# Performance work log

Measured on AMD Instinct MI355X. Metric: run time of the kernel, lower is better.

The kernel has to match this reference:

```python
import jax, jax.numpy as jnp
import numpy as np

N = 100000
NFEAT = 128
NHID = 128
NCLASS = 40
E = 1600000
EPS = 1e-5


def _spmm(vals, src, dst, x, n):
    # y[dst] += vals * x[src]  (sparse adj @ x)
    return jax.ops.segment_sum(vals[:, None] * x[src], dst, num_segments=n)


def _bn(h, gamma, beta, rmean, rvar):
    # BatchNorm1d in eval mode (running statistics)
    return (h - rmean) * jax.lax.rsqrt(rvar + EPS) * gamma + beta


def setup_inputs() -> dict:
    key = jax.random.key(0)
    ks = jax.random.split(key, 24)
    inp = {
        'x': jax.random.normal(ks[0], (N, NFEAT), dtype=jnp.float32),
        'M': jax.random.uniform(ks[1], (N, 1), dtype=jnp.float32),
        'AM': jax.random.uniform(ks[2], (N, 1), dtype=jnp.float32),
        'srcZ': jax.random.randint(ks[3], (E,), 0, N, dtype=jnp.int32),
        'dstZ': jax.random.randint(ks[4], (E,), 0, N, dtype=jnp.int32),
        'valsZ': jax.random.uniform(ks[5], (E,), dtype=jnp.float32),
        'src': jax.random.randint(ks[6], (E,), 0, N, dtype=jnp.int32),
        'dst': jax.random.randint(ks[7], (E,), 0, N, dtype=jnp.int32),
        'vals': jax.random.uniform(ks[8], (E,), dtype=jnp.float32),
        # layer 0 (PaGConv) params
        'W0': jax.random.normal(ks[9], (NHID, NFEAT), dtype=jnp.float32) * (1.414 / np.sqrt(NFEAT)),
        'b0': jnp.zeros((NHID,), dtype=jnp.float32),
        'g0': jnp.ones((NHID,), dtype=jnp.float32),
        'be0': jnp.zeros((NHID,), dtype=jnp.float32),
        'rm0': jax.random.normal(ks[10], (NHID,), dtype=jnp.float32) * 0.1,
        'rv0': jax.random.uniform(ks[11], (NHID,), dtype=jnp.float32) + 0.5,
        # layer 1 (GConv) params
        'W1': jax.random.normal(ks[12], (NHID, NHID), dtype=jnp.float32) * (1.414 / np.sqrt(NHID)),
        'b1': jnp.zeros((NHID,), dtype=jnp.float32),
        'g1': jnp.ones((NHID,), dtype=jnp.float32),
        'be1': jnp.zeros((NHID,), dtype=jnp.float32),
        'rm1': jax.random.normal(ks[13], (NHID,), dtype=jnp.float32) * 0.1,
        'rv1': jax.random.uniform(ks[14], (NHID,), dtype=jnp.float32) + 0.5,
        # layer 2 (GConv) params
        'W2': jax.random.normal(ks[15], (NCLASS, NHID), dtype=jnp.float32) * (1.414 / np.sqrt(NHID)),
        'b2': jnp.zeros((NCLASS,), dtype=jnp.float32),
    }
    return inp


def reference(x, M, AM, srcZ, dstZ, valsZ, src, dst, vals,
              W0, b0, g0, be0, rm0, rv0,
              W1, b1, g1, be1, rm1, rv1,
              W2, b2):
    n = x.shape[0]
    # layer 0: PaGConv with adjZ: fc(spmm(adjZ, M*x) * AM), then BN + ReLU (dropout off in eval)
    h = _spmm(valsZ, srcZ, dstZ, M * x, n) * AM
    h = h @ W0.T + b0
    h = jax.nn.relu(_bn(h, g0, be0, rm0, rv0))
    # layer 1: GConv with adj: fc(spmm(adj, h)), then BN + ReLU
    h = _spmm(vals, src, dst, h, n)
    h = h @ W1.T + b1
    h = jax.nn.relu(_bn(h, g1, be1, rm1, rv1))
    # layer 2: GConv, then log_softmax
    h = _spmm(vals, src, dst, h, n)
    h = h @ W2.T + b2
    return jax.nn.log_softmax(h, axis=-1)
```

## Files before the change

kernel.cpp:

```cpp
#include <hip/hip_runtime.h>
#include <math.h>

#define NFEAT 128
#define NCLS 40
#define KSLOT 48
#define BINROWS 64
#define NBINMAX 1600
#define NBLKC 256
#define CHUNKMAX 6400
#define SEGC 7

typedef short bf16x8 __attribute__((ext_vector_type(8)));
typedef float f32x4 __attribute__((ext_vector_type(4)));

__device__ __forceinline__ float bf2f(unsigned int lo16) {
  return __uint_as_float((lo16 & 0xffffu) << 16);
}
__device__ __forceinline__ unsigned int f2bf(float x) {
  unsigned int u = __float_as_uint(x);
  return (u + 0x7fffu + ((u >> 16) & 1u)) >> 16;
}

__global__ void bn_prep(const float* b0, const float* g0, const float* be0,
                        const float* rm0, const float* rv0,
                        const float* b1, const float* g1, const float* be1,
                        const float* rm1, const float* rv1,
                        float* sc0, float* sh0, float* sc1, float* sh1) {
  int t = threadIdx.x;
  if (t < 128) {
    float s = g0[t] * rsqrtf(rv0[t] + 1e-5f);
    sc0[t] = s;
    sh0[t] = (b0[t] - rm0[t]) * s + be0[t];
  } else {
    int i = t - 128;
    float s = g1[i] * rsqrtf(rv1[i] + 1e-5f);
    sc1[i] = s;
    sh1[i] = (b1[i] - rm1[i]) * s + be1[i];
  }
}

__global__ void convert_xm(const float* __restrict__ x, const float* __restrict__ Mv,
                           unsigned short* __restrict__ xm, int n) {
  int i = blockIdx.x * 256 + threadIdx.x;
  if (i >= n * (NFEAT / 8)) return;
  int row = i >> 4;
  float m = Mv[row];
  const float4* p = (const float4*)(x + (size_t)i * 8);
  float4 v0 = p[0], v1 = p[1];
  unsigned int o0 = f2bf(v0.x * m) | (f2bf(v0.y * m) << 16);
  unsigned int o1 = f2bf(v0.z * m) | (f2bf(v0.w * m) << 16);
  unsigned int o2 = f2bf(v1.x * m) | (f2bf(v1.y * m) << 16);
  unsigned int o3 = f2bf(v1.z * m) | (f2bf(v1.w * m) << 16);
  ((uint4*)xm)[i] = make_uint4(o0, o1, o2, o3);
}

__global__ void convert_w(const float* __restrict__ W0, const float* __restrict__ W1,
                          unsigned short* __restrict__ Wb0, unsigned short* __restrict__ Wb1) {
  int i = blockIdx.x * 256 + threadIdx.x;
  const float* W = (i < 2048) ? W0 : W1;
  unsigned short* Wb = (i < 2048) ? Wb0 : Wb1;
  int j = (i < 2048) ? i : i - 2048;
  const float4* p = (const float4*)(W + (size_t)j * 8);
  float4 v0 = p[0], v1 = p[1];
  unsigned int o0 = f2bf(v0.x) | (f2bf(v0.y) << 16);
  unsigned int o1 = f2bf(v0.z) | (f2bf(v0.w) << 16);
  unsigned int o2 = f2bf(v1.x) | (f2bf(v1.y) << 16);
  unsigned int o3 = f2bf(v1.z) | (f2bf(v1.w) << 16);
  ((uint4*)Wb)[j] = make_uint4(o0, o1, o2, o3);
}

__global__ __launch_bounds__(256) void bin_sort_lds(
    const int* __restrict__ srcZ, const int* __restrict__ dstZ, const float* __restrict__ valsZ,
    const int* __restrict__ srcA, const int* __restrict__ dstA, const float* __restrict__ valsA,
    int2* __restrict__ DrmZ, int2* __restrict__ DrmA,
    int2* __restrict__ binsZ, int2* __restrict__ binsA, int E, int nbin, int chunk) {
  __shared__ int2 stage[CHUNKMAX];
  __shared__ int cur[NBINMAX];
  __shared__ int ps[256];
  const int t = threadIdx.x, k = blockIdx.x;
  const int a = blockIdx.y;
  const int* srcp = a ? srcA : srcZ;
  const int* dstp = a ? dstA : dstZ;
  const float* valp = a ? valsA : valsZ;
  int2* Drm = a ? DrmA : DrmZ;
  int2* binsOut = a ? binsA : binsZ;

  for (int i = t; i < nbin; i += 256) cur[i] = 0;
  __syncthreads();
  const int e0 = k * chunk, e1 = min(E, e0 + chunk);
#pragma unroll 4
  for (int e = e0 + t; e < e1; e += 256) atomicAdd(&cur[dstp[e] >> 6], 1);
  __syncthreads();
  int loc[SEGC], cnt[SEGC];
  int s = 0;
#pragma unroll
  for (int j = 0; j < SEGC; ++j) {
    int i = t * SEGC + j;
    int v = (i < nbin) ? cur[i] : 0;
    loc[j] = s; cnt[j] = v;
    s += v;
  }
  ps[t] = s;
  __syncthreads();
  for (int o = 1; o < 256; o <<= 1) {
    int x = (t >= o) ? ps[t - o] : 0;
    __syncthreads();
    ps[t] += x;
    __syncthreads();
  }
  int ex = ps[t] - s;
#pragma unroll
  for (int j = 0; j < SEGC; ++j) {
    int i = t * SEGC + j;
    if (i < nbin) {
      int o = ex + loc[j];
      Drm[(size_t)k * nbin + i] = make_int2(e0 + o, cnt[j]);
      cur[i] = o;
    }
  }
  __syncthreads();
#pragma unroll 2
  for (int e = e0 + t; e < e1; e += 256) {
    int d = dstp[e];
    int p = atomicAdd(&cur[d >> 6], 1);
    stage[p] = make_int2(srcp[e] | ((d & 63) << 17), __float_as_int(valp[e]));
  }
  __syncthreads();
  const int n = e1 - e0;
  for (int i = t; i < n; i += 256) binsOut[e0 + i] = stage[i];
}

__global__ __launch_bounds__(256) void transposeD(
    const int2* __restrict__ DrmZ, int2* __restrict__ DbmZ,
    const int2* __restrict__ DrmA, int2* __restrict__ DbmA, int nbin) {
  __shared__ int2 st[8][256];
  const int2* Drm = blockIdx.y ? DrmA : DrmZ;
  int2* Dbm = blockIdx.y ? DbmA : DbmZ;
  int t = threadIdx.x;
  int i0 = blockIdx.x * 8;
#pragma unroll
  for (int j = 0; j < 8; ++j) {
    int i = i0 + j;
    st[j][t] = (i < nbin) ? Drm[(size_t)t * nbin + i] : make_int2(0, 0);
  }
  __syncthreads();
  int j = t >> 5, ks = (t & 31) * 8;
  int i = i0 + j;
  if (i < nbin) {
    int2* q = &Dbm[(size_t)i * NBLKC + ks];
#pragma unroll
    for (int m = 0; m < 8; ++m) q[m] = st[j][ks + m];
  }
}

__device__ __forceinline__ void build_slots(const int2* __restrict__ Dbm,
                                            const int2* __restrict__ bins,
                                            int bin, int t,
                                            int2 (*slots)[KSLOT], int* cur) {
  if (t < BINROWS) cur[t] = 0;
  __syncthreads();
  int2 run = Dbm[(size_t)bin * NBLKC + t];
  for (int j = 0; j < run.y; ++j) {
    int2 en = bins[run.x + j];
    int row = (en.x >> 17) & 63;
    int p = atomicAdd(&cur[row], 1);
    if (p < KSLOT) slots[row][p] = make_int2(en.x & 0x1FFFF, en.y);
  }
  __syncthreads();
}

template <bool SCALE>
__global__ __launch_bounds__(256) void spmm128_bin(
    const int2* __restrict__ Dbm, const int2* __restrict__ bins,
    const unsigned short* __restrict__ X, const float* __restrict__ AM,
    unsigned short* __restrict__ Y, int n) {
  __shared__ int2 slots[BINROWS][KSLOT];
  __shared__ int cur[BINROWS];
  int t = threadIdx.x;
  build_slots(Dbm, bins, blockIdx.x, t, slots, cur);

  int wave = t >> 6, lane = t & 63;
  int half = lane >> 5, l32 = lane & 31;
  int row0 = blockIdx.x * BINROWS;

  for (int i = 0; i < 16; ++i) {
    int r = wave * 16 + i;
    int grow = row0 + r;
    if (grow >= n) break;
    int d = min(cur[r], KSLOT);
    int2 my = (lane < d) ? slots[r][lane] : make_int2(0, 0);
    int myc = my.x;
    float myw = __int_as_float(my.y);
    float s0 = 0.f, s1 = 0.f, s2 = 0.f, s3 = 0.f;
    for (int k = 0; k < d; k += 8) {
#pragma unroll
      for (int s = 0; s < 4; ++s) {
        int idx = k + 2 * s + half;
        int c = __shfl(myc, idx);
        float wv = __shfl(myw, idx);
        uint2 pv = *(const uint2*)(X + (size_t)c * NFEAT + l32 * 4);
        s0 += wv * bf2f(pv.x);
        s1 += wv * bf2f(pv.x >> 16);
        s2 += wv * bf2f(pv.y);
        s3 += wv * bf2f(pv.y >> 16);
      }
    }
    s0 += __shfl_xor(s0, 32); s1 += __shfl_xor(s1, 32);
    s2 += __shfl_xor(s2, 32); s3 += __shfl_xor(s3, 32);
    if (SCALE) {
      float am = AM[grow];
      s0 *= am; s1 *= am; s2 *= am; s3 *= am;
    }
    unsigned int pk = half ? (f2bf(s2) | (f2bf(s3) << 16)) : (f2bf(s0) | (f2bf(s1) << 16));
    ((unsigned int*)Y)[(size_t)grow * (NFEAT / 2) + l32 * 2 + half] = pk;
  }
}

__global__ __launch_bounds__(256) void gemm_mfma128(
    const unsigned short* __restrict__ Y, const unsigned short* __restrict__ Wb,
    const float* __restrict__ scale, const float* __restrict__ shift,
    unsigned short* __restrict__ Out, int M) {
  const int wave = threadIdx.x >> 6;
  const int lane = threadIdx.x & 63;
  const int quad = lane >> 4;
  const int l16 = lane & 15;
  const int arow = blockIdx.x * 64 + wave * 16 + l16;
  const bool rv = arow < M;

  f32x4 acc[8];
#pragma unroll
  for (int c = 0; c < 8; ++c) acc[c] = (f32x4){0.f, 0.f, 0.f, 0.f};

#pragma unroll
  for (int kc = 0; kc < 128; kc += 32) {
    bf16x8 a = rv ? *(const bf16x8*)(Y + (size_t)arow * 128 + kc + quad * 8)
                  : (bf16x8){0, 0, 0, 0, 0, 0, 0, 0};
#pragma unroll
    for (int c = 0; c < 8; ++c) {
      bf16x8 b = *(const bf16x8*)(Wb + (size_t)(c * 16 + l16) * 128 + kc + quad * 8);
      acc[c] = __builtin_amdgcn_mfma_f32_16x16x32_bf16(a, b, acc[c], 0, 0, 0);
    }
  }

  int orow0 = blockIdx.x * 64 + wave * 16 + quad * 4;
#pragma unroll
  for (int c = 0; c < 8; ++c) {
    int col = c * 16 + l16;
    float sc = scale[col], sh = shift[col];
#pragma unroll
    for (int r = 0; r < 4; ++r) {
      int orow = orow0 + r;
      if (orow < M) {
        float v = fmaxf(acc[c][r] * sc + sh, 0.f);
        Out[(size_t)orow * 128 + col] = (unsigned short)f2bf(v);
      }
    }
  }
}

__global__ __launch_bounds__(256) void gemm40_kernel(
    const unsigned short* __restrict__ Y, const float* __restrict__ W,
    float* __restrict__ Out, int M, int NoutReal) {
  __shared__ float Yt[16][128];
  __shared__ float Bt[16][64];
  const int t = threadIdx.x;
  const int tx = t & 15, ty = t >> 4;
  const int row0 = blockIdx.x * 128;

  float acc[8][4];
#pragma unroll
  for (int i = 0; i < 8; ++i)
#pragma unroll
    for (int j = 0; j < 4; ++j) acc[i][j] = 0.f;

  for (int kc = 0; kc < 128; kc += 16) {
    {
      int r = t >> 1, kh = (t & 1) * 8;
      int gr = row0 + r;
      uint4 v = make_uint4(0, 0, 0, 0);
      if (gr < M) v = *(const uint4*)(Y + (size_t)gr * 128 + kc + kh);
      unsigned int p;
      p = v.x; Yt[kh + 0][r] = bf2f(p); Yt[kh + 1][r] = bf2f(p >> 16);
      p = v.y; Yt[kh + 2][r] = bf2f(p); Yt[kh + 3][r] = bf2f(p >> 16);
      p = v.z; Yt[kh + 4][r] = bf2f(p); Yt[kh + 5][r] = bf2f(p >> 16);
      p = v.w; Yt[kh + 6][r] = bf2f(p); Yt[kh + 7][r] = bf2f(p >> 16);
    }
    {
      int o = t >> 2, kq = t & 3;
      float4 v = make_float4(0.f, 0.f, 0.f, 0.f);
      if (o < NoutReal) v = *(const float4*)&W[(size_t)o * 128 + kc + kq * 4];
      Bt[kq * 4 + 0][o] = v.x; Bt[kq * 4 + 1][o] = v.y;
      Bt[kq * 4 + 2][o] = v.z; Bt[kq * 4 + 3][o] = v.w;
    }
    __syncthreads();
#pragma unroll
    for (int kk = 0; kk < 16; ++kk) {
      float a[8];
      const float4* ap = (const float4*)(&Yt[kk][ty * 8]);
      float4 a0 = ap[0], a1 = ap[1];
      a[0] = a0.x; a[1] = a0.y; a[2] = a0.z; a[3] = a0.w;
      a[4] = a1.x; a[5] = a1.y; a[6] = a1.z; a[7] = a1.w;
      float4 bv = *(const float4*)(&Bt[kk][tx * 4]);
      float b[4] = {bv.x, bv.y, bv.z, bv.w};
#pragma unroll
      for (int i = 0; i < 8; ++i)
#pragma unroll
        for (int j = 0; j < 4; ++j) acc[i][j] += a[i] * b[j];
    }
    __syncthreads();
  }

#pragma unroll
  for (int i = 0; i < 8; ++i) {
    int gr = row0 + ty * 8 + i;
    if (gr < M) {
#pragma unroll
      for (int j = 0; j < 4; ++j) {
        int col = tx * 4 + j;
        if (col < NoutReal) Out[(size_t)gr * NoutReal + col] = acc[i][j];
      }
    }
  }
}

__global__ __launch_bounds__(256) void spmm_softmax_bin(
    const int2* __restrict__ Dbm, const int2* __restrict__ bins,
    const float* __restrict__ G, const float* __restrict__ b2,
    float* __restrict__ out, int n) {
  __shared__ int2 slots[BINROWS][KSLOT];
  __shared__ int cur[BINROWS];
  int t = threadIdx.x;
  build_slots(Dbm, bins, blockIdx.x, t, slots, cur);

  int wave = t >> 6, lane = t & 63;
  int g = lane / 20;
  int l20 = lane - g * 20;
  bool act = lane < 60;
  int gi = act ? g : 0;
  int row0 = blockIdx.x * BINROWS;
  float b2v0 = b2[l20 * 2], b2v1 = b2[l20 * 2 + 1];

  for (int i = 0; i < 16; ++i) {
    int r = wave * 16 + i;
    int grow = row0 + r;
    if (grow >= n) break;
    int d = min(cur[r], KSLOT);
    int2 my = (lane < d) ? slots[r][lane] : make_int2(0, 0);
    int myc = my.x;
    float myw = __int_as_float(my.y);
    float s0 = 0.f, s1 = 0.f;
    for (int k = 0; k < d; k += 6) {
#pragma unroll
      for (int u = 0; u < 2; ++u) {
        int idx = k + 3 * u + gi;
        int c = __shfl(myc, idx);
        float wv = __shfl(myw, idx);
        if (!act) wv = 0.f;
        float2 gv = *(const float2*)(G + (size_t)c * NCLS + l20 * 2);
        s0 += wv * gv.x;
        s1 += wv * gv.y;
      }
    }
    float r0 = s0 + __shfl(s0, lane + 20) + __shfl(s0, lane + 40);
    float r1 = s1 + __shfl(s1, lane + 20) + __shfl(s1, lane + 40);
    bool v20 = lane < 20;
    float z0 = r0 + b2v0, z1 = r1 + b2v1;
    float m = v20 ? fmaxf(z0, z1) : -INFINITY;
#pragma unroll
    for (int o = 16; o; o >>= 1) m = fmaxf(m, __shfl_xor(m, o));
    float ex = v20 ? (__expf(z0 - m) + __expf(z1 - m)) : 0.f;
#pragma unroll
    for (int o = 16; o; o >>= 1) ex += __shfl_xor(ex, o);
    float lg = m + __logf(ex);
    if (v20) {
      *(float2*)&out[(size_t)grow * NCLS + l20 * 2] = make_float2(z0 - lg, z1 - lg);
    }
  }
}


extern "C" void kernel_launch(void* const* d_in, const int* in_sizes, int n_in,
                              void* d_out, int out_size, void* d_ws, size_t ws_size,
                              hipStream_t stream) {
  const float* x    = (const float*)d_in[0];
  const float* Mv   = (const float*)d_in[1];
  const float* AM   = (const float*)d_in[2];
  const int* srcZ   = (const int*)d_in[3];
  const int* dstZ   = (const int*)d_in[4];
  const float* valsZ= (const float*)d_in[5];
  const int* src    = (const int*)d_in[6];
  const int* dst    = (const int*)d_in[7];
  const float* vals = (const float*)d_in[8];
  const float* W0   = (const float*)d_in[9];
  const float* b0   = (const float*)d_in[10];
  const float* g0   = (const float*)d_in[11];
  const float* be0  = (const float*)d_in[12];
  const float* rm0  = (const float*)d_in[13];
  const float* rv0  = (const float*)d_in[14];
  const float* W1   = (const float*)d_in[15];
  const float* b1   = (const float*)d_in[16];
  const float* g1   = (const float*)d_in[17];
  const float* be1  = (const float*)d_in[18];
  const float* rm1  = (const float*)d_in[19];
  const float* rv1  = (const float*)d_in[20];
  const float* W2   = (const float*)d_in[21];
  const float* b2   = (const float*)d_in[22];
  float* out = (float*)d_out;

  const int N = in_sizes[1];
  const int E = in_sizes[3];
  const int NBIN = (N + BINROWS - 1) / BINROWS;
  const int CHUNK = (E + NBLKC - 1) / NBLKC;

  char* w = (char*)d_ws;
  size_t off = 0;
  auto alloc = [&](size_t bytes) -> void* {
    void* p = w + off;
    off = (off + bytes + 255) & ~(size_t)255;
    return p;
  };
  int2* binsZ = (int2*)alloc((size_t)NBLKC * CHUNK * 8);
  int2* binsA = (int2*)alloc((size_t)NBLKC * CHUNK * 8);
  int2* DrmZ = (int2*)alloc((size_t)NBLKC * NBIN * 8);
  int2* DrmA = (int2*)alloc((size_t)NBLKC * NBIN * 8);
  int2* DbmZ = (int2*)alloc((size_t)NBIN * NBLKC * 8);
  int2* DbmA = (int2*)alloc((size_t)NBIN * NBLKC * 8);
  unsigned short* bufA = (unsigned short*)alloc((size_t)N * NFEAT * 2);
  unsigned short* bufB = (unsigned short*)alloc((size_t)N * NFEAT * 2);
  unsigned short* xm = (unsigned short*)alloc((size_t)N * NFEAT * 2);
  float* sc0 = (float*)alloc(128 * 4);
  float* sh0 = (float*)alloc(128 * 4);
  float* sc1 = (float*)alloc(128 * 4);
  float* sh1 = (float*)alloc(128 * 4);
  unsigned short* Wb0 = (unsigned short*)alloc(128 * 128 * 2);
  unsigned short* Wb1 = (unsigned short*)alloc(128 * 128 * 2);
  float* G2 = (float*)bufA;

  const int GB64 = (N + 63) / 64;
  const int GB128 = (N + 127) / 128;

  bn_prep<<<1, 256, 0, stream>>>(b0, g0, be0, rm0, rv0, b1, g1, be1, rm1, rv1,
                                 sc0, sh0, sc1, sh1);
  convert_xm<<<(N * (NFEAT / 8) + 255) / 256, 256, 0, stream>>>(x, Mv, xm, N);
  convert_w<<<16, 256, 0, stream>>>(W0, W1, Wb0, Wb1);

  bin_sort_lds<<<dim3(NBLKC, 2), 256, 0, stream>>>(srcZ, dstZ, valsZ, src, dst, vals,
                                                   DrmZ, DrmA, binsZ, binsA, E, NBIN, CHUNK);
  transposeD<<<dim3((NBIN + 7) / 8, 2), 256, 0, stream>>>(DrmZ, DbmZ, DrmA, DbmA, NBIN);

  spmm128_bin<true><<<NBIN, 256, 0, stream>>>(DbmZ, binsZ, xm, AM, bufA, N);
  gemm_mfma128<<<GB64, 256, 0, stream>>>(bufA, Wb0, sc0, sh0, bufB, N);

  spmm128_bin<false><<<NBIN, 256, 0, stream>>>(DbmA, binsA, bufB, (const float*)nullptr,
                                               bufA, N);
  gemm_mfma128<<<GB64, 256, 0, stream>>>(bufA, Wb1, sc1, sh1, bufB, N);

  gemm40_kernel<<<GB128, 256, 0, stream>>>(bufB, W2, G2, N, NCLS);
  spmm_softmax_bin<<<NBIN, 256, 0, stream>>>(DbmA, binsA, G2, b2, out, N);
}
```

Before: 586.4 us.

## Build CSR via row sort and use feature-sliced SpMM with bf16 logits

Replaces per-bin LDS slot building inside each SpMM with a separate row_sort pass that produces a CSR (rowptr plus sorted edges) per adjacency. Node features move to a slice-major layout (8 slices of 16 features), and SpMM is launched per slice so each block gathers 32-byte rows that fit better in cache. The final layer stores logits as padded bf16 and the softmax SpMM runs on that. The cost is extra sort kernels, serialized sorting of the two graphs, bf16 rounding of the logits, and aliasing of the Z CSR into bufB.

```diff
diff --git a/kernel.cpp b/kernel.cpp
--- a/kernel.cpp
+++ b/kernel.cpp
@@ -3,12 +3,13 @@
 
 #define NFEAT 128
 #define NCLS 40
-#define KSLOT 48
+#define NCLSP 64
 #define BINROWS 64
 #define NBINMAX 1600
 #define NBLKC 256
 #define CHUNKMAX 6400
 #define SEGC 7
+#define RSMAX 2048
 
 typedef short bf16x8 __attribute__((ext_vector_type(8)));
 typedef float f32x4 __attribute__((ext_vector_type(4)));
@@ -44,14 +45,16 @@
   int i = blockIdx.x * 256 + threadIdx.x;
   if (i >= n * (NFEAT / 8)) return;
   int row = i >> 4;
+  int f0 = (i & 15) * 8;
   float m = Mv[row];
-  const float4* p = (const float4*)(x + (size_t)i * 8);
+  const float4* p = (const float4*)(x + (size_t)row * NFEAT + f0);
   float4 v0 = p[0], v1 = p[1];
-  unsigned int o0 = f2bf(v0.x * m) | (f2bf(v0.y * m) << 16);
-  unsigned int o1 = f2bf(v0.z * m) | (f2bf(v0.w * m) << 16);
-  unsigned int o2 = f2bf(v1.x * m) | (f2bf(v1.y * m) << 16);
-  unsigned int o3 = f2bf(v1.z * m) | (f2bf(v1.w * m) << 16);
-  ((uint4*)xm)[i] = make_uint4(o0, o1, o2, o3);
+  uint4 o;
+  o.x = f2bf(v0.x * m) | (f2bf(v0.y * m) << 16);
+  o.y = f2bf(v0.z * m) | (f2bf(v0.w * m) << 16);
+  o.z = f2bf(v1.x * m) | (f2bf(v1.y * m) << 16);
+  o.w = f2bf(v1.z * m) | (f2bf(v1.w * m) << 16);
+  *(uint4*)(xm + (size_t)(f0 >> 4) * n * 16 + (size_t)row * 16 + (f0 & 8)) = o;
 }
 
 __global__ void convert_w(const float* __restrict__ W0, const float* __restrict__ W1,
@@ -69,22 +72,13 @@
   ((uint4*)Wb)[j] = make_uint4(o0, o1, o2, o3);
 }
 
-__global__ __launch_bounds__(256) void bin_sort_lds(
-    const int* __restrict__ srcZ, const int* __restrict__ dstZ, const float* __restrict__ valsZ,
-    const int* __restrict__ srcA, const int* __restrict__ dstA, const float* __restrict__ valsA,
-    int2* __restrict__ DrmZ, int2* __restrict__ DrmA,
-    int2* __restrict__ binsZ, int2* __restrict__ binsA, int E, int nbin, int chunk) {
+__global__ __launch_bounds__(256) void bin_sort1(
+    const int* __restrict__ srcp, const int* __restrict__ dstp, const float* __restrict__ valp,
+    int2* __restrict__ Drm, int2* __restrict__ binsC, int E, int nbin, int chunk) {
   __shared__ int2 stage[CHUNKMAX];
   __shared__ int cur[NBINMAX];
   __shared__ int ps[256];
   const int t = threadIdx.x, k = blockIdx.x;
-  const int a = blockIdx.y;
-  const int* srcp = a ? srcA : srcZ;
-  const int* dstp = a ? dstA : dstZ;
-  const float* valp = a ? valsA : valsZ;
-  int2* Drm = a ? DrmA : DrmZ;
-  int2* binsOut = a ? binsA : binsZ;
-
   for (int i = t; i < nbin; i += 256) cur[i] = 0;
   __syncthreads();
   const int e0 = k * chunk, e1 = min(E, e0 + chunk);
@@ -127,15 +121,13 @@
   }
   __syncthreads();
   const int n = e1 - e0;
-  for (int i = t; i < n; i += 256) binsOut[e0 + i] = stage[i];
-}
-
-__global__ __launch_bounds__(256) void transposeD(
-    const int2* __restrict__ DrmZ, int2* __restrict__ DbmZ,
-    const int2* __restrict__ DrmA, int2* __restrict__ DbmA, int nbin) {
+  for (int i = t; i < n; i += 256) binsC[e0 + i] = stage[i];
+}
+
+__global__ __launch_bounds__(256) void transposeD1(
+    const int2* __restrict__ Drm, int2* __restrict__ Dbm, int* __restrict__ binTot, int nbin) {
   __shared__ int2 st[8][256];
-  const int2* Drm = blockIdx.y ? DrmA : DrmZ;
-  int2* Dbm = blockIdx.y ? DbmA : DbmZ;
+  __shared__ int part[256];
   int t = threadIdx.x;
   int i0 = blockIdx.x * 8;
 #pragma unroll
@@ -144,82 +136,167 @@
     st[j][t] = (i < nbin) ? Drm[(size_t)t * nbin + i] : make_int2(0, 0);
   }
   __syncthreads();
-  int j = t >> 5, ks = (t & 31) * 8;
-  int i = i0 + j;
-  if (i < nbin) {
-    int2* q = &Dbm[(size_t)i * NBLKC + ks];
-#pragma unroll
-    for (int m = 0; m < 8; ++m) q[m] = st[j][ks + m];
-  }
-}
-
-__device__ __forceinline__ void build_slots(const int2* __restrict__ Dbm,
-                                            const int2* __restrict__ bins,
-                                            int bin, int t,
-                                            int2 (*slots)[KSLOT], int* cur) {
-  if (t < BINROWS) cur[t] = 0;
-  __syncthreads();
-  int2 run = Dbm[(size_t)bin * NBLKC + t];
+  {
+    int j = t >> 5, ks = (t & 31) * 8;
+    int i = i0 + j;
+    if (i < nbin) {
+      int2* q = &Dbm[(size_t)i * NBLKC + ks];
+#pragma unroll
+      for (int m = 0; m < 8; ++m) q[m] = st[j][ks + m];
+    }
+    int p = 0;
+#pragma unroll
+    for (int m = 0; m < 8; ++m) p += st[j][ks + m].y;
+    part[t] = p;
+  }
+  __syncthreads();
+  if (t < 8) {
+    int s = 0;
+    for (int k = 0; k < 32; ++k) s += part[t * 32 + k];
+    if (i0 + t < nbin) binTot[i0 + t] = s;
+  }
+}
+
+__global__ __launch_bounds__(256) void bin_start1(
+    const int* __restrict__ bt, int* __restrict__ bs, int nbin) {
+  __shared__ int ps[256];
+  int t = threadIdx.x;
+  int C = (nbin + 255) / 256;
+  int loc[SEGC + 1];
+  int sum = 0;
+  for (int j = 0; j < C; ++j) {
+    int i = t * C + j;
+    loc[j] = sum;
+    sum += (i < nbin) ? bt[i] : 0;
+  }
+  ps[t] = sum;
+  __syncthreads();
+  for (int o = 1; o < 256; o <<= 1) {
+    int x = (t >= o) ? ps[t - o] : 0;
+    __syncthreads();
+    ps[t] += x;
+    __syncthreads();
+  }
+  int ex = ps[t] - sum;
+  for (int j = 0; j < C; ++j) {
+    int i = t * C + j;
+    if (i < nbin) bs[i] = ex + loc[j];
+  }
+  if (t == 255) bs[nbin] = ps[255];
+}
+
+__global__ __launch_bounds__(256) void row_sort(
+    const int2* __restrict__ Dbm, const int2* __restrict__ binsC,
+    const int* __restrict__ binStart, int2* __restrict__ bins2,
+    int* __restrict__ rowptr, int n, int nbin) {
+  __shared__ int2 stage[RSMAX];
+  __shared__ int ps[256];
+  __shared__ int rcnt[BINROWS];
+  __shared__ int roff[BINROWS];
+  const int b = blockIdx.x, t = threadIdx.x;
+  if (t < BINROWS) rcnt[t] = 0;
+  int2 run = Dbm[(size_t)b * NBLKC + t];
+  ps[t] = run.y;
+  __syncthreads();
+  for (int o = 1; o < 256; o <<= 1) {
+    int x = (t >= o) ? ps[t - o] : 0;
+    __syncthreads();
+    ps[t] += x;
+    __syncthreads();
+  }
+  int mystart = ps[t] - run.y;
   for (int j = 0; j < run.y; ++j) {
-    int2 en = bins[run.x + j];
+    int2 en = binsC[run.x + j];
+    int idx = mystart + j;
+    if (idx < RSMAX) stage[idx] = en;
+    atomicAdd(&rcnt[(en.x >> 17) & 63], 1);
+  }
+  __syncthreads();
+  const int bs = binStart[b];
+  if (t < BINROWS) {
+    int c = rcnt[t];
+    int s = c;
+#pragma unroll
+    for (int o = 1; o < 64; o <<= 1) {
+      int v = __shfl_up(s, o);
+      if (t >= o) s += v;
+    }
+    int excl = s - c;
+    int row = b * BINROWS + t;
+    if (row < n) rowptr[row] = bs + excl;
+    roff[t] = excl;
+  }
+  __syncthreads();
+  int total = min(ps[255], RSMAX);
+  for (int i = t; i < total; i += 256) {
+    int2 en = stage[i];
     int row = (en.x >> 17) & 63;
-    int p = atomicAdd(&cur[row], 1);
-    if (p < KSLOT) slots[row][p] = make_int2(en.x & 0x1FFFF, en.y);
-  }
-  __syncthreads();
+    int p = atomicAdd(&roff[row], 1);
+    bins2[bs + p] = en;
+  }
+  if (b == nbin - 1 && t == 0) rowptr[n] = binStart[nbin];
 }
 
 template <bool SCALE>
-__global__ __launch_bounds__(256) void spmm128_bin(
-    const int2* __restrict__ Dbm, const int2* __restrict__ bins,
-    const unsigned short* __restrict__ X, const float* __restrict__ AM,
-    unsigned short* __restrict__ Y, int n) {
-  __shared__ int2 slots[BINROWS][KSLOT];
-  __shared__ int cur[BINROWS];
-  int t = threadIdx.x;
-  build_slots(Dbm, bins, blockIdx.x, t, slots, cur);
-
-  int wave = t >> 6, lane = t & 63;
-  int half = lane >> 5, l32 = lane & 31;
-  int row0 = blockIdx.x * BINROWS;
+__global__ __launch_bounds__(256) void spmm16_sliced(
+    const int* __restrict__ rowptr, const int2* __restrict__ bins2,
+    const unsigned short* __restrict__ Xp, const float* __restrict__ AM,
+    unsigned short* __restrict__ Yp, int n) {
+  const int slice = blockIdx.x & 7;
+  const int bin = blockIdx.x >> 3;
+  const int t = threadIdx.x;
+  const int wave = t >> 6, lane = t & 63;
+  const int eidx = lane >> 2, q = lane & 3;
+  const unsigned short* Xs = Xp + (size_t)slice * n * 16;
+  unsigned short* Ys = Yp + (size_t)slice * n * 16;
+  const int row0 = bin * BINROWS;
 
   for (int i = 0; i < 16; ++i) {
-    int r = wave * 16 + i;
-    int grow = row0 + r;
-    if (grow >= n) break;
-    int d = min(cur[r], KSLOT);
-    int2 my = (lane < d) ? slots[r][lane] : make_int2(0, 0);
-    int myc = my.x;
-    float myw = __int_as_float(my.y);
-    float s0 = 0.f, s1 = 0.f, s2 = 0.f, s3 = 0.f;
-    for (int k = 0; k < d; k += 8) {
-#pragma unroll
-      for (int s = 0; s < 4; ++s) {
-        int idx = k + 2 * s + half;
+    int row = row0 + wave * 16 + i;
+    if (row >= n) break;
+    int s0 = rowptr[row], d = rowptr[row + 1] - s0;
+    float a0 = 0.f, a1 = 0.f, a2 = 0.f, a3 = 0.f;
+    for (int kb = 0; kb < d; kb += 64) {
+      int rem = min(64, d - kb);
+      int2 my = (lane < rem) ? bins2[s0 + kb + lane] : make_int2(0, 0);
+      int myc = my.x & 0x1FFFF;
+      float myw = __int_as_float(my.y);
+      int steps = (rem + 15) >> 4;
+      for (int st = 0; st < steps; ++st) {
+        int idx = st * 16 + eidx;
         int c = __shfl(myc, idx);
         float wv = __shfl(myw, idx);
-        uint2 pv = *(const uint2*)(X + (size_t)c * NFEAT + l32 * 4);
-        s0 += wv * bf2f(pv.x);
-        s1 += wv * bf2f(pv.x >> 16);
-        s2 += wv * bf2f(pv.y);
-        s3 += wv * bf2f(pv.y >> 16);
+        uint2 pv = *(const uint2*)(Xs + (size_t)c * 16 + q * 4);
+        a0 += wv * bf2f(pv.x);
+        a1 += wv * bf2f(pv.x >> 16);
+        a2 += wv * bf2f(pv.y);
+        a3 += wv * bf2f(pv.y >> 16);
       }
     }
-    s0 += __shfl_xor(s0, 32); s1 += __shfl_xor(s1, 32);
-    s2 += __shfl_xor(s2, 32); s3 += __shfl_xor(s3, 32);
+#pragma unroll
+    for (int m = 4; m < 64; m <<= 1) {
+      a0 += __shfl_xor(a0, m);
+      a1 += __shfl_xor(a1, m);
+      a2 += __shfl_xor(a2, m);
+      a3 += __shfl_xor(a3, m);
+    }
     if (SCALE) {
-      float am = AM[grow];
-      s0 *= am; s1 *= am; s2 *= am; s3 *= am;
-    }
-    unsigned int pk = half ? (f2bf(s2) | (f2bf(s3) << 16)) : (f2bf(s0) | (f2bf(s1) << 16));
-    ((unsigned int*)Y)[(size_t)grow * (NFEAT / 2) + l32 * 2 + half] = pk;
+      float am = AM[row];
+      a0 *= am; a1 *= am; a2 *= am; a3 *= am;
+    }
+    if (lane < 4) {
+      uint2 pk;
+      pk.x = f2bf(a0) | (f2bf(a1) << 16);
+      pk.y = f2bf(a2) | (f2bf(a3) << 16);
+      *(uint2*)(Ys + (size_t)row * 16 + lane * 4) = pk;
+    }
   }
 }
 
 __global__ __launch_bounds__(256) void gemm_mfma128(
-    const unsigned short* __restrict__ Y, const unsigned short* __restrict__ Wb,
+    const unsigned short* __restrict__ Yp, const unsigned short* __restrict__ Wb,
     const float* __restrict__ scale, const float* __restrict__ shift,
-    unsigned short* __restrict__ Out, int M) {
+    unsigned short* __restrict__ Outp, int M) {
   const int wave = threadIdx.x >> 6;
   const int lane = threadIdx.x & 63;
   const int quad = lane >> 4;
@@ -233,7 +310,8 @@
 
 #pragma unroll
   for (int kc = 0; kc < 128; kc += 32) {
-    bf16x8 a = rv ? *(const bf16x8*)(Y + (size_t)arow * 128 + kc + quad * 8)
+    int f = kc + quad * 8;
+    bf16x8 a = rv ? *(const bf16x8*)(Yp + (size_t)(f >> 4) * M * 16 + (size_t)arow * 16 + (f & 8))
                   : (bf16x8){0, 0, 0, 0, 0, 0, 0, 0};
 #pragma unroll
     for (int c = 0; c < 8; ++c) {
@@ -247,20 +325,21 @@
   for (int c = 0; c < 8; ++c) {
     int col = c * 16 + l16;
     float sc = scale[col], sh = shift[col];
+    unsigned short* Op = Outp + (size_t)c * M * 16;
 #pragma unroll
     for (int r = 0; r < 4; ++r) {
       int orow = orow0 + r;
       if (orow < M) {
         float v = fmaxf(acc[c][r] * sc + sh, 0.f);
-        Out[(size_t)orow * 128 + col] = (unsigned short)f2bf(v);
+        Op[(size_t)orow * 16 + l16] = (unsigned short)f2bf(v);
       }
     }
   }
 }
 
 __global__ __launch_bounds__(256) void gemm40_kernel(
-    const unsigned short* __restrict__ Y, const float* __restrict__ W,
-    float* __restrict__ Out, int M, int NoutReal) {
+    const unsigned short* __restrict__ Yp, const float* __restrict__ W,
+    unsigned short* __restrict__ G2, int M, int NoutReal) {
   __shared__ float Yt[16][128];
   __shared__ float Bt[16][64];
   const int t = threadIdx.x;
@@ -277,8 +356,9 @@
     {
       int r = t >> 1, kh = (t & 1) * 8;
       int gr = row0 + r;
+      int f = kc + kh;
       uint4 v = make_uint4(0, 0, 0, 0);
-      if (gr < M) v = *(const uint4*)(Y + (size_t)gr * 128 + kc + kh);
+      if (gr < M) v = *(const uint4*)(Yp + (size_t)(f >> 4) * M * 16 + (size_t)gr * 16 + (f & 8));
       unsigned int p;
       p = v.x; Yt[kh + 0][r] = bf2f(p); Yt[kh + 1][r] = bf2f(p >> 16);
       p = v.y; Yt[kh + 2][r] = bf2f(p); Yt[kh + 3][r] = bf2f(p >> 16);
@@ -314,66 +394,63 @@
   for (int i = 0; i < 8; ++i) {
     int gr = row0 + ty * 8 + i;
     if (gr < M) {
-#pragma unroll
-      for (int j = 0; j < 4; ++j) {
-        int col = tx * 4 + j;
-        if (col < NoutReal) Out[(size_t)gr * NoutReal + col] = acc[i][j];
-      }
-    }
-  }
-}
-
-__global__ __launch_bounds__(256) void spmm_softmax_bin(
-    const int2* __restrict__ Dbm, const int2* __restrict__ bins,
-    const float* __restrict__ G, const float* __restrict__ b2,
+      uint2 pk;
+      pk.x = f2bf(acc[i][0]) | (f2bf(acc[i][1]) << 16);
+      pk.y = f2bf(acc[i][2]) | (f2bf(acc[i][3]) << 16);
+      *(uint2*)(G2 + (size_t)gr * NCLSP + tx * 4) = pk;
+    }
+  }
+}
+
+__global__ __launch_bounds__(256) void spmm_softmax64(
+    const int* __restrict__ rowptr, const int2* __restrict__ bins2,
+    const unsigned short* __restrict__ G2, const float* __restrict__ b2,
     float* __restrict__ out, int n) {
-  __shared__ int2 slots[BINROWS][KSLOT];
-  __shared__ int cur[BINROWS];
-  int t = threadIdx.x;
-  build_slots(Dbm, bins, blockIdx.x, t, slots, cur);
-
-  int wave = t >> 6, lane = t & 63;
-  int g = lane / 20;
-  int l20 = lane - g * 20;
-  bool act = lane < 60;
-  int gi = act ? g : 0;
-  int row0 = blockIdx.x * BINROWS;
-  float b2v0 = b2[l20 * 2], b2v1 = b2[l20 * 2 + 1];
+  const int t = threadIdx.x;
+  const int wave = t >> 6, lane = t & 63;
+  const int eidx = lane >> 4, q = lane & 15;
+  const int row0 = blockIdx.x * BINROWS;
+  const bool vq = q < (NCLS / 4);
+  float4 bv = vq ? *(const float4*)(b2 + q * 4) : make_float4(0.f, 0.f, 0.f, 0.f);
 
   for (int i = 0; i < 16; ++i) {
-    int r = wave * 16 + i;
-    int grow = row0 + r;
-    if (grow >= n) break;
-    int d = min(cur[r], KSLOT);
-    int2 my = (lane < d) ? slots[r][lane] : make_int2(0, 0);
-    int myc = my.x;
-    float myw = __int_as_float(my.y);
-    float s0 = 0.f, s1 = 0.f;
-    for (int k = 0; k < d; k += 6) {
-#pragma unroll
-      for (int u = 0; u < 2; ++u) {
-        int idx = k + 3 * u + gi;
+    int row = row0 + wave * 16 + i;
+    if (row >= n) break;
+    int s0 = rowptr[row], d = rowptr[row + 1] - s0;
+    float a0 = 0.f, a1 = 0.f, a2 = 0.f, a3 = 0.f;
+    for (int kb = 0; kb < d; kb += 64) {
+      int rem = min(64, d - kb);
+      int2 my = (lane < rem) ? bins2[s0 + kb + lane] : make_int2(0, 0);
+      int myc = my.x & 0x1FFFF;
+      float myw = __int_as_float(my.y);
+      int steps = (rem + 3) >> 2;
+      for (int st = 0; st < steps; ++st) {
+        int idx = st * 4 + eidx;
         int c = __shfl(myc, idx);
         float wv = __shfl(myw, idx);
-        if (!act) wv = 0.f;
-        float2 gv = *(const float2*)(G + (size_t)c * NCLS + l20 * 2);
-        s0 += wv * gv.x;
-        s1 += wv * gv.y;
+        uint2 pv = *(const uint2*)(G2 + (size_t)c * NCLSP + q * 4);
+        a0 += wv * bf2f(pv.x);
+        a1 += wv * bf2f(pv.x >> 16);
+        a2 += wv * bf2f(pv.y);
+        a3 += wv * bf2f(pv.y >> 16);
       }
     }
-    float r0 = s0 + __shfl(s0, lane + 20) + __shfl(s0, lane + 40);
-    float r1 = s1 + __shfl(s1, lane + 20) + __shfl(s1, lane + 40);
-    bool v20 = lane < 20;
-    float z0 = r0 + b2v0, z1 = r1 + b2v1;
-    float m = v20 ? fmaxf(z0, z1) : -INFINITY;
-#pragma unroll
-    for (int o = 16; o; o >>= 1) m = fmaxf(m, __shfl_xor(m, o));
-    float ex = v20 ? (__expf(z0 - m) + __expf(z1 - m)) : 0.f;
-#pragma unroll
-    for (int o = 16; o; o >>= 1) ex += __shfl_xor(ex, o);
+    a0 += __shfl_xor(a0, 16); a1 += __shfl_xor(a1, 16);
+    a2 += __shfl_xor(a2, 16); a3 += __shfl_xor(a3, 16);
+    a0 += __shfl_xor(a0, 32); a1 += __shfl_xor(a1, 32);
+    a2 += __shfl_xor(a2, 32); a3 += __shfl_xor(a3, 32);
+    float z0 = a0 + bv.x, z1 = a1 + bv.y, z2 = a2 + bv.z, z3 = a3 + bv.w;
+    bool par = (eidx == 0) && vq;
+    float m = par ? fmaxf(fmaxf(z0, z1), fmaxf(z2, z3)) : -INFINITY;
+#pragma unroll
+    for (int o = 1; o < 64; o <<= 1) m = fmaxf(m, __shfl_xor(m, o));
+    float ex = par ? (__expf(z0 - m) + __expf(z1 - m) + __expf(z2 - m) + __expf(z3 - m)) : 0.f;
+#pragma unroll
+    for (int o = 1; o < 64; o <<= 1) ex += __shfl_xor(ex, o);
     float lg = m + __logf(ex);
-    if (v20) {
-      *(float2*)&out[(size_t)grow * NCLS + l20 * 2] = make_float2(z0 - lg, z1 - lg);
+    if (par) {
+      *(float4*)&out[(size_t)row * NCLS + q * 4] =
+          make_float4(z0 - lg, z1 - lg, z2 - lg, z3 - lg);
     }
   }
 }
@@ -419,42 +496,52 @@
     off = (off + bytes + 255) & ~(size_t)255;
     return p;
   };
-  int2* binsZ = (int2*)alloc((size_t)NBLKC * CHUNK * 8);
-  int2* binsA = (int2*)alloc((size_t)NBLKC * CHUNK * 8);
-  int2* DrmZ = (int2*)alloc((size_t)NBLKC * NBIN * 8);
-  int2* DrmA = (int2*)alloc((size_t)NBLKC * NBIN * 8);
-  int2* DbmZ = (int2*)alloc((size_t)NBIN * NBLKC * 8);
-  int2* DbmA = (int2*)alloc((size_t)NBIN * NBLKC * 8);
+  int2* binsC = (int2*)alloc((size_t)NBLKC * CHUNK * 8);
+  int2* Drm = (int2*)alloc((size_t)NBLKC * NBIN * 8);
+  int2* Dbm = (int2*)alloc((size_t)NBIN * NBLKC * 8);
+  int* binTot = (int*)alloc((size_t)NBIN * 4);
+  int* binStart = (int*)alloc((size_t)(NBIN + 1) * 4);
+  int2* bins2A = (int2*)alloc((size_t)E * 8);
+  int* rowptrA = (int*)alloc((size_t)(N + 1) * 4);
+  unsigned short* xm = (unsigned short*)alloc((size_t)N * NFEAT * 2);
   unsigned short* bufA = (unsigned short*)alloc((size_t)N * NFEAT * 2);
   unsigned short* bufB = (unsigned short*)alloc((size_t)N * NFEAT * 2);
-  unsigned short* xm = (unsigned short*)alloc((size_t)N * NFEAT * 2);
   float* sc0 = (float*)alloc(128 * 4);
   float* sh0 = (float*)alloc(128 * 4);
   float* sc1 = (float*)alloc(128 * 4);
   float* sh1 = (float*)alloc(128 * 4);
   unsigned short* Wb0 = (unsigned short*)alloc(128 * 128 * 2);
   unsigned short* Wb1 = (unsigned short*)alloc(128 * 128 * 2);
-  float* G2 = (float*)bufA;
+  int2* bins2Z = (int2*)bufB;
+  int* rowptrZ = (int*)((char*)bufB + 13 * 1024 * 1024);
+  unsigned short* G2 = bufA;
 
   const int GB64 = (N + 63) / 64;
   const int GB128 = (N + 127) / 128;
+  const int TDB = (NBIN + 7) / 8;
 
   bn_prep<<<1, 256, 0, stream>>>(b0, g0, be0, rm0, rv0, b1, g1, be1, rm1, rv1,
                                  sc0, sh0, sc1, sh1);
   convert_xm<<<(N * (NFEAT / 8) + 255) / 256, 256, 0, stream>>>(x, Mv, xm, N);
   convert_w<<<16, 256, 0, stream>>>(W0, W1, Wb0, Wb1);
 
-  bin_sort_lds<<<dim3(NBLKC, 2), 256, 0, stream>>>(srcZ, dstZ, valsZ, src, dst, vals,
-                                                   DrmZ, DrmA, binsZ, binsA, E, NBIN, CHUNK);
-  transposeD<<<dim3((NBIN + 7) / 8, 2), 256, 0, stream>>>(DrmZ, DbmZ, DrmA, DbmA, NBIN);
-
-  spmm128_bin<true><<<NBIN, 256, 0, stream>>>(DbmZ, binsZ, xm, AM, bufA, N);
+  bin_sort1<<<NBLKC, 256, 0, stream>>>(srcZ, dstZ, valsZ, Drm, binsC, E, NBIN, CHUNK);
+  transposeD1<<<TDB, 256, 0, stream>>>(Drm, Dbm, binTot, NBIN);
+  bin_start1<<<1, 256, 0, stream>>>(binTot, binStart, NBIN);
+  row_sort<<<NBIN, 256, 0, stream>>>(Dbm, binsC, binStart, bins2Z, rowptrZ, N, NBIN);
+
+  bin_sort1<<<NBLKC, 256, 0, stream>>>(src, dst, vals, Drm, binsC, E, NBIN, CHUNK);
+  transposeD1<<<TDB, 256, 0, stream>>>(Drm, Dbm, binTot, NBIN);
+  bin_start1<<<1, 256, 0, stream>>>(binTot, binStart, NBIN);
+  row_sort<<<NBIN, 256, 0, stream>>>(Dbm, binsC, binStart, bins2A, rowptrA, N, NBIN);
+
+  spmm16_sliced<true><<<NBIN * 8, 256, 0, stream>>>(rowptrZ, bins2Z, xm, AM, bufA, N);
   gemm_mfma128<<<GB64, 256, 0, stream>>>(bufA, Wb0, sc0, sh0, bufB, N);
 
-  spmm128_bin<false><<<NBIN, 256, 0, stream>>>(DbmA, binsA, bufB, (const float*)nullptr,
-                                               bufA, N);
+  spmm16_sliced<false><<<NBIN * 8, 256, 0, stream>>>(rowptrA, bins2A, bufB,
+                                                     (const float*)nullptr, bufA, N);
   gemm_mfma128<<<GB64, 256, 0, stream>>>(bufA, Wb1, sc1, sh1, bufB, N);
 
   gemm40_kernel<<<GB128, 256, 0, stream>>>(bufB, W2, G2, N, NCLS);
-  spmm_softmax_bin<<<NBIN, 256, 0, stream>>>(DbmA, binsA, G2, b2, out, N);
-}
+  spmm_softmax64<<<NBIN, 256, 0, stream>>>(rowptrA, bins2A, G2, b2, out, N);
+}
```

Measured after the change: 844.2 us. 1.44x slower.
